# Performance work log

Measured on AMD Instinct MI355X. Metric: run time of the kernel, lower is better.

## Reference

```python
import jax, jax.numpy as jnp
import numpy as np

N = 300000
IN_C = 64
OUT_C = 128
N_Z = 8
B, H, W = 4, 256, 256


def setup_inputs() -> dict:
    key = jax.random.key(0)
    k = jax.random.split(key, 7)
    std = 1.0 / np.sqrt(IN_C)
    return {
        "features": jax.random.normal(k[0], (N, IN_C), dtype=jnp.float32),
        "kernel": jax.random.uniform(k[1], (N_Z, IN_C, OUT_C), dtype=jnp.float32, minval=-std, maxval=std),
        "bias": jnp.zeros((1, OUT_C), dtype=jnp.float32),
        "batch_idx": jax.random.randint(k[2], (N,), 0, B, dtype=jnp.int32),
        "d0_idx": jax.random.randint(k[3], (N,), 0, H, dtype=jnp.int32),
        "d1_idx": jax.random.randint(k[4], (N,), 0, W, dtype=jnp.int32),
        "z_idx": jax.random.randint(k[5], (N,), 0, N_Z, dtype=jnp.int32),
    }


def reference(features, kernel, bias, batch_idx, d0_idx, d1_idx, z_idx):
    # stride s = 1 on the drcv path, so //s is identity
    z = jnp.clip(z_idx, 0, N_Z - 1)
    flat_bev = batch_idx * (H * W) + d0_idx * W + d1_idx  # [N]
    # per-point learned matmul: features[n] @ kernel[z[n]]
    # (computed as a small fixed loop over n_z height bins to avoid
    #  materializing the [N, in_c, out_c] gathered kernel)
    bev_feat = jnp.zeros((features.shape[0], OUT_C), dtype=features.dtype)
    for zz in range(N_Z):
        bev_feat = bev_feat + jnp.where((z == zz)[:, None], features @ kernel[zz], 0.0)
    bev_feat = bev_feat + bias
    # scatter_add into dense BEV
    bev = jnp.zeros((B * H * W, OUT_C), dtype=features.dtype).at[flat_bev].add(bev_feat)
    return bev.reshape(B, H, W, OUT_C).transpose(0, 3, 1, 2)
```

## Files before the change

### kernel.cpp

```cpp
#include <hip/hip_runtime.h>

#define PPB   128
#define NZ    8
#define INC   64
#define OUTC  128
#define NB    4
#define HH    256
#define WWD   256
#define HWD   (HH * WWD)
#define NSEG  (NB * HH)
#define NCELL (NB * HH * WWD)

typedef __attribute__((ext_vector_type(8))) short bf16x8;
typedef __attribute__((ext_vector_type(4))) float f32x4;

__device__ __forceinline__ unsigned bf16_rne(float x) {
    unsigned u = __float_as_uint(x);
    return (u + 0x7FFFu + ((u >> 16) & 1u)) >> 16;
}
__device__ __forceinline__ unsigned pack2(float lo, float hi) {
    return bf16_rne(lo) | (bf16_rne(hi) << 16);
}

__global__ void hist_kernel(const int* __restrict__ z_idx, const int* __restrict__ batch_idx,
                            const int* __restrict__ d0_idx, const int* __restrict__ d1_idx,
                            int* __restrict__ counts, int* __restrict__ cellhist, int n) {
    __shared__ int lc[NZ];
    int t = threadIdx.x;
    if (t < NZ) lc[t] = 0;
    __syncthreads();
    int i = blockIdx.x * blockDim.x + t;
    if (i < n) {
        int z = z_idx[i]; z = z < 0 ? 0 : (z > NZ - 1 ? NZ - 1 : z);
        atomicAdd(&lc[z], 1);
        int cell = (batch_idx[i] * HH + d0_idx[i]) * WWD + d1_idx[i];
        atomicAdd(&cellhist[cell], 1);
    }
    __syncthreads();
    if (t < NZ && lc[t] > 0) atomicAdd(&counts[t], lc[t]);
}

__global__ void prefix_z_kernel(const int* __restrict__ counts, int* __restrict__ pstart) {
    if (threadIdx.x == 0 && blockIdx.x == 0) {
        int off = 0;
        for (int z = 0; z < NZ; ++z) {
            pstart[z] = off;
            off += ((counts[z] + PPB - 1) / PPB) * PPB;
        }
        pstart[NZ] = off;
    }
}

__global__ __launch_bounds__(256) void scan_local(const int* __restrict__ cellhist,
                                                  int* __restrict__ cellstart,
                                                  int* __restrict__ chunksum) {
    __shared__ int ts[256];
    int t = threadIdx.x;
    int base = blockIdx.x * 1024 + t * 4;
    int4 v = *(const int4*)&cellhist[base];
    int s = v.x + v.y + v.z + v.w;
    ts[t] = s;
    __syncthreads();
    for (int d = 1; d < 256; d <<= 1) {
        int x = (t >= d) ? ts[t - d] : 0;
        __syncthreads();
        ts[t] += x;
        __syncthreads();
    }
    int excl = ts[t] - s;
    int4 o;
    o.x = excl; o.y = excl + v.x; o.z = o.y + v.y; o.w = o.z + v.z;
    *(int4*)&cellstart[base] = o;
    if (t == 255) chunksum[blockIdx.x] = ts[255];
}

__global__ __launch_bounds__(256) void scan_top(int* __restrict__ chunksum,
                                                int* __restrict__ cellstart) {
    __shared__ int ts[256];
    int t = threadIdx.x;
    int s = chunksum[t];
    ts[t] = s;
    __syncthreads();
    for (int d = 1; d < 256; d <<= 1) {
        int x = (t >= d) ? ts[t - d] : 0;
        __syncthreads();
        ts[t] += x;
        __syncthreads();
    }
    chunksum[t] = ts[t] - s;
    if (t == 255) cellstart[NCELL] = ts[255];
}

__global__ __launch_bounds__(256) void scan_add(int* __restrict__ cellstart,
                                                const int* __restrict__ chunksum) {
    int off = chunksum[blockIdx.x];
    if (off == 0) return;
    int base = blockIdx.x * 1024 + threadIdx.x * 4;
    int4 v = *(int4*)&cellstart[base];
    v.x += off; v.y += off; v.z += off; v.w += off;
    *(int4*)&cellstart[base] = v;
}

__global__ void scatter_kernel(const int* __restrict__ z_idx, const int* __restrict__ batch_idx,
                               const int* __restrict__ d0_idx, const int* __restrict__ d1_idx,
                               const int* __restrict__ pstart, int* __restrict__ cursors,
                               const int* __restrict__ cellstart, int* __restrict__ cellcur,
                               int* __restrict__ bins, int* __restrict__ segpos, int n) {
    __shared__ int lc[NZ];
    __shared__ int lbase[NZ];
    int t = threadIdx.x;
    if (t < NZ) lc[t] = 0;
    __syncthreads();
    int i = blockIdx.x * blockDim.x + t;
    int z = 0, rank = 0;
    bool valid = (i < n);
    if (valid) {
        z = z_idx[i]; z = z < 0 ? 0 : (z > NZ - 1 ? NZ - 1 : z);
        rank = atomicAdd(&lc[z], 1);
    }
    __syncthreads();
    if (t < NZ) lbase[t] = (lc[t] > 0) ? atomicAdd(&cursors[t], lc[t]) : 0;
    __syncthreads();
    if (valid) {
        int slot = pstart[z] + lbase[z] + rank;
        bins[slot] = i;
        int cell = (batch_idx[i] * HH + d0_idx[i]) * WWD + d1_idx[i];
        int r2 = atomicAdd(&cellcur[cell], 1);
        segpos[slot] = 1 + cellstart[cell] + r2;
    }
}

__global__ __launch_bounds__(256) void gemm_kernel(
        const float* __restrict__ features, const float* __restrict__ kw,
        const float* __restrict__ bias,
        const int* __restrict__ pstart, const int* __restrict__ bins,
        const int* __restrict__ segpos, unsigned* __restrict__ bevf) {
    __shared__ __align__(16) char lbuf[32768];
    __shared__ int psl[PPB];
    char* Abf = lbuf;
    char* Wbf = lbuf + 16384;

    int start = blockIdx.x * PPB;
    int total = pstart[NZ];
    if (start >= total) return;
    int z = 0;
#pragma unroll
    for (int zz = 1; zz < NZ; ++zz)
        if (start >= pstart[zz]) z = zz;

    int tid = threadIdx.x;
    if (tid < PPB) psl[tid] = segpos[start + tid];

    {
        int r = tid >> 1, half = tid & 1;
        int raw = bins[start + r];
        int nid = raw < 0 ? 0 : raw;
        const float4* fp = (const float4*)(features + (size_t)nid * INC) + half * 8;
        float4 f[8];
#pragma unroll
        for (int q = 0; q < 8; ++q) f[q] = fp[q];
        unsigned u[16];
#pragma unroll
        for (int m = 0; m < 8; ++m) {
            u[2 * m]     = pack2(f[m].x, f[m].y);
            u[2 * m + 1] = pack2(f[m].z, f[m].w);
        }
#pragma unroll
        for (int ch = 0; ch < 4; ++ch) {
            int off = (r * 128 + half * 64 + ch * 16) ^ ((r & 7) << 4);
            uint4 val = make_uint4(u[4 * ch], u[4 * ch + 1], u[4 * ch + 2], u[4 * ch + 3]);
            *(uint4*)(Abf + off) = val;
        }
    }
    {
        int c = tid & 127, kh = tid >> 7;
        const float* wp = kw + (size_t)z * INC * OUTC + c;
        float wv[32];
#pragma unroll
        for (int j = 0; j < 32; ++j) wv[j] = wp[(size_t)(kh * 32 + j) * OUTC];
        unsigned u[16];
#pragma unroll
        for (int m = 0; m < 16; ++m) u[m] = pack2(wv[2 * m], wv[2 * m + 1]);
#pragma unroll
        for (int ch = 0; ch < 4; ++ch) {
            int off = (c * 128 + kh * 64 + ch * 16) ^ ((c & 7) << 4);
            uint4 val = make_uint4(u[4 * ch], u[4 * ch + 1], u[4 * ch + 2], u[4 * ch + 3]);
            *(uint4*)(Wbf + off) = val;
        }
    }
    __syncthreads();

    int wv_ = tid >> 6, l = tid & 63;
    int wr = wv_ >> 1, wc = wv_ & 1;

    f32x4 acc[4][4];
#pragma unroll
    for (int i = 0; i < 4; ++i)
#pragma unroll
        for (int j = 0; j < 4; ++j) acc[i][j] = (f32x4){0.f, 0.f, 0.f, 0.f};

#pragma unroll
    for (int kc = 0; kc < 2; ++kc) {
        bf16x8 af[4], bfr[4];
#pragma unroll
        for (int pb = 0; pb < 4; ++pb) {
            int p = wr * 64 + pb * 16 + (l & 15);
            int off = (p * 128 + kc * 64 + (l >> 4) * 16) ^ ((p & 7) << 4);
            af[pb] = *(const bf16x8*)(Abf + off);
        }
#pragma unroll
        for (int cb = 0; cb < 4; ++cb) {
            int c = wc * 64 + cb * 16 + (l & 15);
            int off = (c * 128 + kc * 64 + (l >> 4) * 16) ^ ((c & 7) << 4);
            bfr[cb] = *(const bf16x8*)(Wbf + off);
        }
#pragma unroll
        for (int pb = 0; pb < 4; ++pb)
#pragma unroll
            for (int cb = 0; cb < 4; ++cb)
                acc[pb][cb] = __builtin_amdgcn_mfma_f32_16x16x32_bf16(
                    af[pb], bfr[cb], acc[pb][cb], 0, 0, 0);
    }
    __syncthreads();

    float bias_c[4];
#pragma unroll
    for (int cb = 0; cb < 4; ++cb) bias_c[cb] = bias[wc * 64 + cb * 16 + (l & 15)];

#pragma unroll
    for (int pb = 0; pb < 4; ++pb) {
#pragma unroll
        for (int cb = 0; cb < 4; ++cb) {
            int c = wc * 64 + cb * 16 + (l & 15);
#pragma unroll
            for (int q = 0; q < 4; ++q) {
                int prow = wr * 64 + pb * 16 + (l >> 4) * 4 + q;
                float v = acc[pb][cb][q] + bias_c[cb];
                int byteoff = (prow * 256 + c * 2) ^ (((prow >> 2) & 3) << 5);
                *(unsigned short*)(lbuf + byteoff) = (unsigned short)bf16_rne(v);
            }
        }
    }
    __syncthreads();

#pragma unroll
    for (int j = 0; j < 8; ++j) {
        int s = j * 256 + tid;
        int prow = s >> 4, chunk = s & 15;
        int byteoff = (prow * 256 + chunk * 16) ^ (((prow >> 2) & 3) << 5);
        uint4 val = *(const uint4*)(lbuf + byteoff);
        int pos = psl[prow];
        *((uint4*)(bevf + (size_t)pos * 64) + chunk) = val;
    }
}

__global__ __launch_bounds__(512) void reduce_kernel(
        const unsigned* __restrict__ bevf, const int* __restrict__ cellstart,
        float* __restrict__ out) {
    __shared__ unsigned tile[256 * 64];
    int t = threadIdx.x;
    int blk = blockIdx.x;
    blk = (blk & 7) * (NSEG / 8) + (blk >> 3);
    int seg = blk;
    int wv = t >> 6, l = t & 63;

    int cell0 = seg * WWD + wv * 32;
    int cs_n = cellstart[cell0];
    int ce_n = cellstart[cell0 + 1];
    for (int j = 0; j < 32; ++j) {
        int cs = cs_n, ce = ce_n;
        cs_n = ce;
        if (j < 31) ce_n = cellstart[cell0 + j + 2];
        float f0 = 0.f, f1 = 0.f;
        int k = cs;
        for (; k + 1 < ce; k += 2) {
            unsigned v0 = bevf[(size_t)(k + 1) * 64 + l];
            unsigned v1 = bevf[(size_t)(k + 2) * 64 + l];
            f0 += __uint_as_float(v0 << 16);
            f1 += __uint_as_float(v0 & 0xFFFF0000u);
            f0 += __uint_as_float(v1 << 16);
            f1 += __uint_as_float(v1 & 0xFFFF0000u);
        }
        if (k < ce) {
            unsigned v0 = bevf[(size_t)(k + 1) * 64 + l];
            f0 += __uint_as_float(v0 << 16);
            f1 += __uint_as_float(v0 & 0xFFFF0000u);
        }
        int w = wv * 32 + j;
        tile[w * 64 + ((l + w) & 63)] = pack2(f0, f1);
    }
    __syncthreads();

    int b = seg >> 8, h = seg & 255;
    float* ob = out + (size_t)b * OUTC * HWD + (size_t)h * WWD;
#pragma unroll
    for (int r = 0; r < 16; ++r) {
        int c = wv + 8 * r;
        int d = c >> 1;
        float* op = ob + (size_t)c * HWD;
#pragma unroll
        for (int q = 0; q < 4; ++q) {
            int w = 64 * q + l;
            unsigned v = tile[w * 64 + ((d + w) & 63)];
            op[w] = __uint_as_float((c & 1) ? (v & 0xFFFF0000u) : (v << 16));
        }
    }
}

__global__ __launch_bounds__(256) void naive_kernel(
        const float* __restrict__ features, const float* __restrict__ kw,
        const float* __restrict__ bias,
        const int* __restrict__ bidx, const int* __restrict__ d0,
        const int* __restrict__ d1, const int* __restrict__ zi,
        float* __restrict__ out, int n) {
    long long gid = (long long)blockIdx.x * blockDim.x + threadIdx.x;
    int pid = (int)(gid >> 7);
    int c   = (int)(gid & (OUTC - 1));
    if (pid >= n) return;
    int z = zi[pid]; z = z < 0 ? 0 : (z > NZ - 1 ? NZ - 1 : z);
    const float4* fp = (const float4*)(features + (size_t)pid * INC);
    const float* wp = kw + (size_t)z * INC * OUTC + c;
    float a0 = bias[c], a1 = 0.f, a2 = 0.f, a3 = 0.f;
#pragma unroll
    for (int i = 0; i < INC / 4; ++i) {
        float4 f = fp[i];
        a0 += f.x * wp[(size_t)(4 * i + 0) * OUTC];
        a1 += f.y * wp[(size_t)(4 * i + 1) * OUTC];
        a2 += f.z * wp[(size_t)(4 * i + 2) * OUTC];
        a3 += f.w * wp[(size_t)(4 * i + 3) * OUTC];
    }
    float acc = (a0 + a1) + (a2 + a3);
    size_t oidx = ((size_t)bidx[pid] * OUTC + c) * HWD + (size_t)d0[pid] * WWD + d1[pid];
    unsafeAtomicAdd(&out[oidx], acc);
}

extern "C" void kernel_launch(void* const* d_in, const int* in_sizes, int n_in,
                              void* d_out, int out_size, void* d_ws, size_t ws_size,
                              hipStream_t stream) {
    const float* features = (const float*)d_in[0];
    const float* kw       = (const float*)d_in[1];
    const float* bias     = (const float*)d_in[2];
    const int* batch_idx  = (const int*)d_in[3];
    const int* d0_idx     = (const int*)d_in[4];
    const int* d1_idx     = (const int*)d_in[5];
    const int* z_idx      = (const int*)d_in[6];
    float* out = (float*)d_out;
    int n = in_sizes[0] / INC;

    size_t binsElems = (size_t)n + (size_t)NZ * PPB;
    size_t bevfBytes = (binsElems + 1) * OUTC * 2;
    size_t metaOff   = (bevfBytes + 255) & ~(size_t)255;
    size_t chOff     = metaOff + 32 * 4;
    size_t ccOff     = chOff + (size_t)NCELL * 4;
    size_t csOff     = ccOff + (size_t)NCELL * 4;
    size_t ckOff     = csOff + (size_t)(NCELL + 4) * 4;
    size_t binsOff   = (ckOff + 256 * 4 + 255) & ~(size_t)255;
    size_t posOff    = binsOff + binsElems * 4;
    size_t need      = posOff + binsElems * 4 + 16;

    if (ws_size >= need) {
        char* ws = (char*)d_ws;
        unsigned* bevf = (unsigned*)ws;
        int* meta      = (int*)(ws + metaOff);
        int* counts    = meta;
        int* cursors   = meta + 8;
        int* pstart    = meta + 16;
        int* cellhist  = (int*)(ws + chOff);
        int* cellcur   = (int*)(ws + ccOff);
        int* cellstart = (int*)(ws + csOff);
        int* chunksum  = (int*)(ws + ckOff);
        int* bins      = (int*)(ws + binsOff);
        int* segpos    = (int*)(ws + posOff);

        hipMemsetAsync(meta, 0, 32 * 4, stream);
        hipMemsetAsync(cellhist, 0, (size_t)NCELL * 4, stream);
        hipMemsetAsync(cellcur, 0, (size_t)NCELL * 4, stream);
        hipMemsetAsync(bins, 0xFF, binsElems * 4, stream);
        hipMemsetAsync(segpos, 0, binsElems * 4, stream);

        int gb = (n + 255) / 256;
        hist_kernel<<<gb, 256, 0, stream>>>(z_idx, batch_idx, d0_idx, d1_idx,
                                            counts, cellhist, n);
        prefix_z_kernel<<<1, 64, 0, stream>>>(counts, pstart);
        scan_local<<<256, 256, 0, stream>>>(cellhist, cellstart, chunksum);
        scan_top<<<1, 256, 0, stream>>>(chunksum, cellstart);
        scan_add<<<256, 256, 0, stream>>>(cellstart, chunksum);
        scatter_kernel<<<gb, 256, 0, stream>>>(z_idx, batch_idx, d0_idx, d1_idx,
                                               pstart, cursors, cellstart, cellcur,
                                               bins, segpos, n);

        int nblk = (int)((binsElems + PPB - 1) / PPB) + 1;
        gemm_kernel<<<nblk, 256, 0, stream>>>(features, kw, bias, pstart, bins,
                                              segpos, bevf);

        reduce_kernel<<<NSEG, 512, 0, stream>>>(bevf, cellstart, out);
    } else {
        hipMemsetAsync(out, 0, (size_t)out_size * sizeof(float), stream);
        long long threads = (long long)n * OUTC;
        int gb = (int)((threads + 255) / 256);
        naive_kernel<<<gb, 256, 0, stream>>>(features, kw, bias, batch_idx, d0_idx,
                                             d1_idx, z_idx, out, n);
    }
}
```

Before: 173.3 us.

## Prepack bf16 weights, drop cellcur and memsets, merge prefix into scan

```diff
diff --git a/kernel.cpp b/kernel.cpp
--- a/kernel.cpp
+++ b/kernel.cpp
@@ -22,6 +22,22 @@
     return bf16_rne(lo) | (bf16_rne(hi) << 16);
 }
 
+__global__ __launch_bounds__(256) void wprep_kernel(const float* __restrict__ kw,
+                                                    unsigned short* __restrict__ wt) {
+    int z = blockIdx.x;
+    const float* src = kw + (size_t)z * INC * OUTC;
+    unsigned short* dst = wt + (size_t)z * OUTC * INC;
+    int t = threadIdx.x;
+    for (int c = t; c < OUTC; c += 256) {
+#pragma unroll
+        for (int k = 0; k < INC; k += 2) {
+            float a = src[(size_t)k * OUTC + c];
+            float b = src[(size_t)(k + 1) * OUTC + c];
+            *(unsigned*)&dst[(size_t)c * INC + k] = pack2(a, b);
+        }
+    }
+}
+
 __global__ void hist_kernel(const int* __restrict__ z_idx, const int* __restrict__ batch_idx,
                             const int* __restrict__ d0_idx, const int* __restrict__ d1_idx,
                             int* __restrict__ counts, int* __restrict__ cellhist, int n) {
@@ -40,17 +56,6 @@
     if (t < NZ && lc[t] > 0) atomicAdd(&counts[t], lc[t]);
 }
 
-__global__ void prefix_z_kernel(const int* __restrict__ counts, int* __restrict__ pstart) {
-    if (threadIdx.x == 0 && blockIdx.x == 0) {
-        int off = 0;
-        for (int z = 0; z < NZ; ++z) {
-            pstart[z] = off;
-            off += ((counts[z] + PPB - 1) / PPB) * PPB;
-        }
-        pstart[NZ] = off;
-    }
-}
-
 __global__ __launch_bounds__(256) void scan_local(const int* __restrict__ cellhist,
                                                   int* __restrict__ cellstart,
                                                   int* __restrict__ chunksum) {
@@ -75,9 +80,18 @@
 }
 
 __global__ __launch_bounds__(256) void scan_top(int* __restrict__ chunksum,
-                                                int* __restrict__ cellstart) {
+                                                const int* __restrict__ counts,
+                                                int* __restrict__ pstart) {
     __shared__ int ts[256];
     int t = threadIdx.x;
+    if (t == 0) {
+        int off = 0;
+        for (int z = 0; z < NZ; ++z) {
+            pstart[z] = off;
+            off += ((counts[z] + PPB - 1) / PPB) * PPB;
+        }
+        pstart[NZ] = off;
+    }
     int s = chunksum[t];
     ts[t] = s;
     __syncthreads();
@@ -88,7 +102,6 @@
         __syncthreads();
     }
     chunksum[t] = ts[t] - s;
-    if (t == 255) cellstart[NCELL] = ts[255];
 }
 
 __global__ __launch_bounds__(256) void scan_add(int* __restrict__ cellstart,
@@ -101,10 +114,22 @@
     *(int4*)&cellstart[base] = v;
 }
 
+__global__ void pad_kernel(const int* __restrict__ counts, const int* __restrict__ pstart,
+                           int* __restrict__ bins, int* __restrict__ segpos) {
+    int z = blockIdx.x;
+    int cnt = counts[z];
+    int s0 = pstart[z];
+    int padded = pstart[z + 1] - s0;
+    for (int i = cnt + threadIdx.x; i < padded; i += blockDim.x) {
+        bins[s0 + i] = -1;
+        segpos[s0 + i] = 0;
+    }
+}
+
 __global__ void scatter_kernel(const int* __restrict__ z_idx, const int* __restrict__ batch_idx,
                                const int* __restrict__ d0_idx, const int* __restrict__ d1_idx,
                                const int* __restrict__ pstart, int* __restrict__ cursors,
-                               const int* __restrict__ cellstart, int* __restrict__ cellcur,
+                               int* __restrict__ cellstart,
                                int* __restrict__ bins, int* __restrict__ segpos, int n) {
     __shared__ int lc[NZ];
     __shared__ int lbase[NZ];
@@ -125,13 +150,13 @@
         int slot = pstart[z] + lbase[z] + rank;
         bins[slot] = i;
         int cell = (batch_idx[i] * HH + d0_idx[i]) * WWD + d1_idx[i];
-        int r2 = atomicAdd(&cellcur[cell], 1);
-        segpos[slot] = 1 + cellstart[cell] + r2;
+        int r2 = atomicAdd(&cellstart[cell], 1);
+        segpos[slot] = 1 + r2;
     }
 }
 
 __global__ __launch_bounds__(256) void gemm_kernel(
-        const float* __restrict__ features, const float* __restrict__ kw,
+        const float* __restrict__ features, const unsigned short* __restrict__ wt,
         const float* __restrict__ bias,
         const int* __restrict__ pstart, const int* __restrict__ bins,
         const int* __restrict__ segpos, unsigned* __restrict__ bevf) {
@@ -173,19 +198,13 @@
         }
     }
     {
-        int c = tid & 127, kh = tid >> 7;
-        const float* wp = kw + (size_t)z * INC * OUTC + c;
-        float wv[32];
-#pragma unroll
-        for (int j = 0; j < 32; ++j) wv[j] = wp[(size_t)(kh * 32 + j) * OUTC];
-        unsigned u[16];
-#pragma unroll
-        for (int m = 0; m < 16; ++m) u[m] = pack2(wv[2 * m], wv[2 * m + 1]);
-#pragma unroll
-        for (int ch = 0; ch < 4; ++ch) {
-            int off = (c * 128 + kh * 64 + ch * 16) ^ ((c & 7) << 4);
-            uint4 val = make_uint4(u[4 * ch], u[4 * ch + 1], u[4 * ch + 2], u[4 * ch + 3]);
-            *(uint4*)(Wbf + off) = val;
+        const uint4* src = (const uint4*)(wt + (size_t)z * OUTC * INC);
+#pragma unroll
+        for (int i = 0; i < 4; ++i) {
+            int s = tid + 256 * i;
+            int c = s >> 3, ch = s & 7;
+            int off = (c * 128 + ch * 16) ^ ((c & 7) << 4);
+            *(uint4*)(Wbf + off) = src[s];
         }
     }
     __syncthreads();
@@ -265,29 +284,41 @@
     int wv = t >> 6, l = t & 63;
 
     int cell0 = seg * WWD + wv * 32;
-    int cs_n = cellstart[cell0];
-    int ce_n = cellstart[cell0 + 1];
-    for (int j = 0; j < 32; ++j) {
-        int cs = cs_n, ce = ce_n;
-        cs_n = ce;
-        if (j < 31) ce_n = cellstart[cell0 + j + 2];
-        float f0 = 0.f, f1 = 0.f;
-        int k = cs;
-        for (; k + 1 < ce; k += 2) {
-            unsigned v0 = bevf[(size_t)(k + 1) * 64 + l];
-            unsigned v1 = bevf[(size_t)(k + 2) * 64 + l];
-            f0 += __uint_as_float(v0 << 16);
-            f1 += __uint_as_float(v0 & 0xFFFF0000u);
-            f0 += __uint_as_float(v1 << 16);
-            f1 += __uint_as_float(v1 & 0xFFFF0000u);
-        }
-        if (k < ce) {
-            unsigned v0 = bevf[(size_t)(k + 1) * 64 + l];
-            f0 += __uint_as_float(v0 << 16);
-            f1 += __uint_as_float(v0 & 0xFFFF0000u);
-        }
+    int idx = cell0 + l - 1;
+    int bound = 0;
+    if (l <= 32) bound = (idx < 0) ? 0 : cellstart[idx];
+    int r0 = __shfl(bound, 0);
+    int r1 = __shfl(bound, 32);
+
+    int j = 0;
+    int ce = __shfl(bound, 1);
+    float f0 = 0.f, f1 = 0.f;
+    for (int r = r0; r < r1; r += 4) {
+        unsigned v[4];
+#pragma unroll
+        for (int u = 0; u < 4; ++u) {
+            int rr = (r + u < r1) ? r + u : r1 - 1;
+            v[u] = bevf[(size_t)(rr + 1) * 64 + l];
+        }
+#pragma unroll
+        for (int u = 0; u < 4; ++u) {
+            if (r + u >= r1) break;
+            while (r + u >= ce) {
+                int w = wv * 32 + j;
+                tile[w * 64 + ((l + w) & 63)] = pack2(f0, f1);
+                f0 = 0.f; f1 = 0.f;
+                ++j;
+                ce = __shfl(bound, j + 1);
+            }
+            f0 += __uint_as_float(v[u] << 16);
+            f1 += __uint_as_float(v[u] & 0xFFFF0000u);
+        }
+    }
+    while (j < 32) {
         int w = wv * 32 + j;
         tile[w * 64 + ((l + w) & 63)] = pack2(f0, f1);
+        f0 = 0.f; f1 = 0.f;
+        ++j;
     }
     __syncthreads();
 
@@ -349,10 +380,10 @@
 
     size_t binsElems = (size_t)n + (size_t)NZ * PPB;
     size_t bevfBytes = (binsElems + 1) * OUTC * 2;
-    size_t metaOff   = (bevfBytes + 255) & ~(size_t)255;
-    size_t chOff     = metaOff + 32 * 4;
-    size_t ccOff     = chOff + (size_t)NCELL * 4;
-    size_t csOff     = ccOff + (size_t)NCELL * 4;
+    size_t wtOff     = (bevfBytes + 255) & ~(size_t)255;
+    size_t metaOff   = wtOff + (size_t)NZ * OUTC * INC * 2;
+    size_t chOff     = (metaOff + 32 * 4 + 255) & ~(size_t)255;
+    size_t csOff     = chOff + (size_t)NCELL * 4;
     size_t ckOff     = csOff + (size_t)(NCELL + 4) * 4;
     size_t binsOff   = (ckOff + 256 * 4 + 255) & ~(size_t)255;
     size_t posOff    = binsOff + binsElems * 4;
@@ -361,12 +392,12 @@
     if (ws_size >= need) {
         char* ws = (char*)d_ws;
         unsigned* bevf = (unsigned*)ws;
+        unsigned short* wt = (unsigned short*)(ws + wtOff);
         int* meta      = (int*)(ws + metaOff);
         int* counts    = meta;
         int* cursors   = meta + 8;
         int* pstart    = meta + 16;
         int* cellhist  = (int*)(ws + chOff);
-        int* cellcur   = (int*)(ws + ccOff);
         int* cellstart = (int*)(ws + csOff);
         int* chunksum  = (int*)(ws + ckOff);
         int* bins      = (int*)(ws + binsOff);
@@ -374,23 +405,21 @@
 
         hipMemsetAsync(meta, 0, 32 * 4, stream);
         hipMemsetAsync(cellhist, 0, (size_t)NCELL * 4, stream);
-        hipMemsetAsync(cellcur, 0, (size_t)NCELL * 4, stream);
-        hipMemsetAsync(bins, 0xFF, binsElems * 4, stream);
-        hipMemsetAsync(segpos, 0, binsElems * 4, stream);
 
         int gb = (n + 255) / 256;
+        wprep_kernel<<<NZ, 256, 0, stream>>>(kw, wt);
         hist_kernel<<<gb, 256, 0, stream>>>(z_idx, batch_idx, d0_idx, d1_idx,
                                             counts, cellhist, n);
-        prefix_z_kernel<<<1, 64, 0, stream>>>(counts, pstart);
         scan_local<<<256, 256, 0, stream>>>(cellhist, cellstart, chunksum);
-        scan_top<<<1, 256, 0, stream>>>(chunksum, cellstart);
+        scan_top<<<1, 256, 0, stream>>>(chunksum, counts, pstart);
         scan_add<<<256, 256, 0, stream>>>(cellstart, chunksum);
+        pad_kernel<<<NZ, 128, 0, stream>>>(counts, pstart, bins, segpos);
         scatter_kernel<<<gb, 256, 0, stream>>>(z_idx, batch_idx, d0_idx, d1_idx,
-                                               pstart, cursors, cellstart, cellcur,
+                                               pstart, cursors, cellstart,
                                                bins, segpos, n);
 
         int nblk = (int)((binsElems + PPB - 1) / PPB) + 1;
-        gemm_kernel<<<nblk, 256, 0, stream>>>(features, kw, bias, pstart, bins,
+        gemm_kernel<<<nblk, 256, 0, stream>>>(features, wt, bias, pstart, bins,
                                               segpos, bevf);
 
         reduce_kernel<<<NSEG, 512, 0, stream>>>(bevf, cellstart, out);
```

Measured after the change: 154.5 us. -10.8%, faster.
